# Kernel tuning notes

Measured on AMD Instinct MI355X. Metric: run time of the kernel, lower is better.

## Reference

```python
import jax, jax.numpy as jnp
import numpy as np

D_MODEL = 1024
NUM_HEADS = 16
D_HEAD = D_MODEL // NUM_HEADS


def setup_inputs() -> dict:
    key = jax.random.key(0)
    ks = jax.random.split(key, 9)
    s = 1.0 / np.sqrt(D_MODEL)
    inp = {"x": jax.random.normal(ks[0], (2, 2048, D_MODEL), dtype=jnp.float32)}
    for i, name in enumerate(["q", "k", "v", "o"]):
        inp[f"W_{name}"] = jax.random.uniform(ks[1 + 2 * i], (D_MODEL, D_MODEL), minval=-s, maxval=s, dtype=jnp.float32)
        inp[f"b_{name}"] = jax.random.uniform(ks[2 + 2 * i], (D_MODEL,), minval=-s, maxval=s, dtype=jnp.float32)
    return inp


def reference(x, W_q, b_q, W_k, b_k, W_v, b_v, W_o, b_o):
    B, S, _ = x.shape
    def heads(W, b):
        # [B,S,D] @ [D,D] -> [B,S,H,Dh] -> [B,H,S,Dh]
        return (x @ W.T + b).reshape(B, S, NUM_HEADS, D_HEAD).transpose(0, 2, 1, 3)
    Q, K, V = heads(W_q, b_q), heads(W_k, b_k), heads(W_v, b_v)
    scores = jnp.einsum("bhqd,bhkd->bhqk", Q, K) / jnp.sqrt(jnp.float32(D_HEAD))
    causal = jnp.tril(jnp.ones((S, S), dtype=bool))  # True = keep
    scores = jnp.where(causal, scores, -jnp.inf)
    A = jax.nn.softmax(scores, axis=-1)
    out = jnp.einsum("bhqk,bhkd->bhqd", A, V)  # [B,H,S,Dh]
    out = out.transpose(0, 2, 1, 3).reshape(B, S, D_MODEL)
    return out @ W_o.T + b_o
```

## Files before the change

### kernel.cpp

```cpp
#include <hip/hip_runtime.h>
#include <math.h>

#define D_MODEL 1024
#define NUM_HEADS 16
#define D_HEAD 64
#define SEQ 2048
#define BATCH 2
#define NROWS (BATCH * SEQ)

typedef short s8v __attribute__((ext_vector_type(8)));
typedef float f4v __attribute__((ext_vector_type(4)));

__device__ __forceinline__ short to_bf(float f) {
    union { float f; unsigned u; } x; x.f = f;
    unsigned r = x.u + 0x7fffu + ((x.u >> 16) & 1u);
    return (short)(r >> 16);
}

__device__ __forceinline__ void gld_lds16(const short* g, short* l) {
    __builtin_amdgcn_global_load_lds(
        (const __attribute__((address_space(1))) unsigned*)g,
        (__attribute__((address_space(3))) unsigned*)l, 16, 0, 0);
}

#define QSCALE 0.180336880f

__global__ __launch_bounds__(256) void cvt_fused(
    const float* __restrict__ x,  const float* __restrict__ Wq,
    const float* __restrict__ Wk, const float* __restrict__ Wv,
    const float* __restrict__ Wo,
    short* __restrict__ Xb, short* __restrict__ Wqkvb, short* __restrict__ Wob)
{
    const int NX = NROWS * D_MODEL / 4;
    const int NW = D_MODEL * D_MODEL / 4;
    int j = blockIdx.x * 256 + threadIdx.x;
    const float* src; short* dst; float sc = 1.f;
    if (j < NX)                 { src = x;  dst = Xb; }
    else if ((j -= NX) < NW)    { src = Wq; dst = Wqkvb; sc = QSCALE; }
    else if ((j -= NW) < NW)    { src = Wk; dst = Wqkvb + NW * 4; }
    else if ((j -= NW) < NW)    { src = Wv; dst = Wqkvb + NW * 8; }
    else                        { j -= NW; src = Wo; dst = Wob; }
    float4 v = ((const float4*)src)[j];
    short4 s = { to_bf(v.x * sc), to_bf(v.y * sc), to_bf(v.z * sc), to_bf(v.w * sc) };
    ((short4*)dst)[j] = s;
}

__global__ __launch_bounds__(256) void gemm_bf16(
    const short* __restrict__ Xb, const short* __restrict__ Wb,
    const float* __restrict__ B0, const float* __restrict__ B1, const float* __restrict__ B2,
    float* __restrict__ Ofp,
    short* __restrict__ Q0, short* __restrict__ K1, short* __restrict__ V2,
    int qkv_mode)
{
    __shared__ __align__(16) short smem[18432];
    short* As = smem;
    short* Bs = smem + 8192;

    const int t    = threadIdx.x;
    const int w    = t >> 6;
    const int lane = t & 63;
    const int quad = lane >> 4;
    const int l15  = lane & 15;
    const int wm   = w & 1, wn = w >> 1;

    const int n0 = blockIdx.x * 128;
    const int m0 = blockIdx.y * 128;

    f4v acc[4][4];
#pragma unroll
    for (int i = 0; i < 4; ++i)
#pragma unroll
        for (int j = 0; j < 4; ++j) acc[i][j] = (f4v){0.f, 0.f, 0.f, 0.f};

    for (int k0 = 0; k0 < D_MODEL; k0 += 64) {
#pragma unroll
        for (int i = 0; i < 4; ++i) {
            const int cid = i * 256 + t;
            const int row = cid >> 3, kc = cid & 7;
            gld_lds16(&Xb[(size_t)(m0 + row) * D_MODEL + k0 + kc * 8],
                      &As[(i * 256 + w * 64) * 8]);
            gld_lds16(&Wb[(size_t)(n0 + row) * D_MODEL + k0 + kc * 8],
                      &Bs[(i * 256 + w * 64) * 8]);
        }
        __syncthreads();

#pragma unroll
        for (int c = 0; c < 2; ++c) {
            s8v af[4], bf[4];
#pragma unroll
            for (int mi = 0; mi < 4; ++mi)
                af[mi] = *(const s8v*)&As[(wm * 64 + mi * 16 + l15) * 64 + c * 32 + quad * 8];
#pragma unroll
            for (int ni = 0; ni < 4; ++ni)
                bf[ni] = *(const s8v*)&Bs[(wn * 64 + ni * 16 + l15) * 64 + c * 32 + quad * 8];
#pragma unroll
            for (int mi = 0; mi < 4; ++mi)
#pragma unroll
                for (int ni = 0; ni < 4; ++ni)
                    acc[mi][ni] = __builtin_amdgcn_mfma_f32_16x16x32_bf16(
                        af[mi], bf[ni], acc[mi][ni], 0, 0, 0);
        }
        __syncthreads();
    }

    if (!qkv_mode) {
#pragma unroll
        for (int ni = 0; ni < 4; ++ni) {
            const int col = n0 + wn * 64 + ni * 16 + l15;
            const float bv = B0[col];
#pragma unroll
            for (int mi = 0; mi < 4; ++mi)
#pragma unroll
                for (int r = 0; r < 4; ++r) {
                    const int row = m0 + wm * 64 + mi * 16 + quad * 4 + r;
                    Ofp[(size_t)row * D_MODEL + col] = acc[mi][ni][r] + bv;
                }
        }
        return;
    }

    const int sel = n0 >> 10;
    const float* bias = sel == 0 ? B0 : sel == 1 ? B1 : B2;
    short* out        = sel == 0 ? Q0 : sel == 1 ? K1 : V2;
    const float bsc   = sel == 0 ? QSCALE : 1.f;
    const int h0 = (n0 & 1023) >> 6;

#pragma unroll
    for (int ni = 0; ni < 4; ++ni) {
        const int col = wn * 64 + ni * 16 + l15;
        const float bv = bias[(n0 & 1023) + col] * bsc;
#pragma unroll
        for (int mi = 0; mi < 4; ++mi)
#pragma unroll
            for (int r = 0; r < 4; ++r) {
                const int row = wm * 64 + mi * 16 + quad * 4 + r;
                const short v = to_bf(acc[mi][ni][r] + bv);
                if (sel < 2) smem[row * 144 + col] = v;
                else         smem[col * 144 + row] = v;
            }
    }
    __syncthreads();

    const int rr = t >> 1, half = t & 1;
    const int bb = m0 >> 11, mloc = m0 & (SEQ - 1);
    const short* src = &smem[rr * 144 + half * 64];
    short* dst;
    if (sel < 2)
        dst = out + (((size_t)(bb * NUM_HEADS + h0 + half) * SEQ + (mloc + rr)) * D_HEAD);
    else
        dst = out + ((size_t)(bb * NUM_HEADS + h0 + (rr >> 6)) * D_HEAD + (rr & 63)) * SEQ
                  + mloc + half * 64;
#pragma unroll
    for (int i = 0; i < 8; ++i)
        ((int4*)dst)[i] = ((const int4*)src)[i];
}

__global__ __launch_bounds__(256) void attn_mfma(
    const short* __restrict__ Qg, const short* __restrict__ Kg,
    const short* __restrict__ Vg, short* __restrict__ ctxb)
{
    __shared__ __align__(16) short Kb[128 * 64];
    __shared__ __align__(16) short Vs[64 * 128];
    __shared__ __align__(16) short Ps[4][32 * 72];
    __shared__ float lbuf[4][36];

    const int t    = threadIdx.x;
    const int w    = t >> 6;
    const int lane = t & 63;
    const int quad = lane >> 4;
    const int l15  = lane & 15;

    const int bidx = blockIdx.x;
    const int p    = bidx & 255;
    const int bh   = p >> 3;
    const int pair = p & 7;
    const int qt   = (bidx < 256) ? pair : 15 - pair;
    const int b    = bh >> 4, h = bh & 15;

    const short* qbase = Qg + (size_t)bh * SEQ * D_HEAD;
    const short* kbase = Kg + (size_t)bh * SEQ * D_HEAD;
    const short* vbase = Vg + (size_t)bh * D_HEAD * SEQ;
    const int q0 = qt * 128;
    const int qw = w * 32;

    s8v aq[2][2];
#pragma unroll
    for (int ns = 0; ns < 2; ++ns)
#pragma unroll
        for (int c = 0; c < 2; ++c)
            aq[ns][c] = *(const s8v*)&qbase[(size_t)(q0 + qw + ns * 16 + l15) * D_HEAD
                                            + c * 32 + quad * 8];

    f4v Oacc[2][4];
#pragma unroll
    for (int ms = 0; ms < 2; ++ms)
#pragma unroll
        for (int nt = 0; nt < 4; ++nt) Oacc[ms][nt] = (f4v){0.f, 0.f, 0.f, 0.f};
    float lsum[2] = {0.f, 0.f};

    for (int j = 0; j <= qt; ++j) {
        __syncthreads();
        {
            const int k0 = j * 128;
#pragma unroll
            for (int i = 0; i < 4; ++i) {
                const int cid = i * 256 + w * 64 + lane;
                {
                    const int row = cid >> 3, pp = cid & 7, g = pp ^ (row & 7);
                    gld_lds16(&kbase[(size_t)(k0 + row) * D_HEAD + g * 8],
                              &Kb[(i * 256 + w * 64) * 8]);
                }
                {
                    const int row = cid >> 4, pp = cid & 15;
                    const int g = (pp & 8) | ((pp & 7) ^ (row & 7));
                    gld_lds16(&vbase[(size_t)row * SEQ + k0 + g * 8],
                              &Vs[(i * 256 + w * 64) * 8]);
                }
            }
        }
        __syncthreads();

        const bool diag = (j == qt);

#pragma unroll
        for (int half = 0; half < 2; ++half) {
#pragma unroll
            for (int mt = 0; mt < 4; ++mt) {
                const int krow = half * 64 + mt * 16 + l15;
                s8v ka0 = *(const s8v*)&Kb[(krow * 8 + (quad ^ (l15 & 7))) * 8];
                s8v ka1 = *(const s8v*)&Kb[(krow * 8 + ((4 + quad) ^ (l15 & 7))) * 8];
#pragma unroll
                for (int ns = 0; ns < 2; ++ns) {
                    f4v st = (f4v){0.f, 0.f, 0.f, 0.f};
                    st = __builtin_amdgcn_mfma_f32_16x16x32_bf16(ka0, aq[ns][0], st, 0, 0, 0);
                    st = __builtin_amdgcn_mfma_f32_16x16x32_bf16(ka1, aq[ns][1], st, 0, 0, 0);
                    if (diag) {
#pragma unroll
                        for (int r = 0; r < 4; ++r)
                            if (half * 64 + mt * 16 + quad * 4 + r > qw + ns * 16 + l15)
                                st[r] = -INFINITY;
                    }
                    float e0 = exp2f(st[0]), e1 = exp2f(st[1]);
                    float e2 = exp2f(st[2]), e3 = exp2f(st[3]);
                    lsum[ns] += (e0 + e1) + (e2 + e3);
                    int2 pk;
                    pk.x = (int)((__float_as_uint(e0) >> 16) | (__float_as_uint(e1) & 0xffff0000u));
                    pk.y = (int)((__float_as_uint(e2) >> 16) | (__float_as_uint(e3) & 0xffff0000u));
                    *(int2*)&Ps[w][(ns * 16 + l15) * 72 + mt * 16 + quad * 4] = pk;
                }
            }
#pragma unroll
            for (int c2 = 0; c2 < 2; ++c2) {
                s8v ap0 = *(const s8v*)&Ps[w][l15 * 72 + c2 * 32 + quad * 8];
                s8v ap1 = *(const s8v*)&Ps[w][(16 + l15) * 72 + c2 * 32 + quad * 8];
                const int g = (half * 2 + c2) * 4 + quad;
                const int pos = (g & 8) | ((g & 7) ^ (l15 & 7));
                s8v bv[4];
#pragma unroll
                for (int nt = 0; nt < 4; ++nt)
                    bv[nt] = *(const s8v*)&Vs[((nt * 16 + l15) * 16 + pos) * 8];
#pragma unroll
                for (int nt = 0; nt < 4; ++nt) {
                    Oacc[0][nt] = __builtin_amdgcn_mfma_f32_16x16x32_bf16(
                        ap0, bv[nt], Oacc[0][nt], 0, 0, 0);
                    Oacc[1][nt] = __builtin_amdgcn_mfma_f32_16x16x32_bf16(
                        ap1, bv[nt], Oacc[1][nt], 0, 0, 0);
                }
            }
        }
    }

#pragma unroll
    for (int ns = 0; ns < 2; ++ns) {
        lsum[ns] += __shfl_xor(lsum[ns], 16, 64);
        lsum[ns] += __shfl_xor(lsum[ns], 32, 64);
    }
    if (quad == 0) { lbuf[w][l15] = lsum[0]; lbuf[w][16 + l15] = lsum[1]; }
#pragma unroll
    for (int ms = 0; ms < 2; ++ms) {
        float4 lv = *(float4*)&lbuf[w][ms * 16 + quad * 4];
        const float li[4] = {lv.x, lv.y, lv.z, lv.w};
#pragma unroll
        for (int r = 0; r < 4; ++r) {
            const float inv = 1.f / li[r];
            const int n = b * SEQ + q0 + qw + ms * 16 + quad * 4 + r;
            short* dst = &ctxb[(size_t)n * D_MODEL + h * D_HEAD + l15];
#pragma unroll
            for (int nt = 0; nt < 4; ++nt)
                dst[nt * 16] = to_bf(Oacc[ms][nt][r] * inv);
        }
    }
}

extern "C" void kernel_launch(void* const* d_in, const int* in_sizes, int n_in,
                              void* d_out, int out_size, void* d_ws, size_t ws_size,
                              hipStream_t stream)
{
    const float* x  = (const float*)d_in[0];
    const float* Wq = (const float*)d_in[1];
    const float* bq = (const float*)d_in[2];
    const float* Wk = (const float*)d_in[3];
    const float* bk = (const float*)d_in[4];
    const float* Wv = (const float*)d_in[5];
    const float* bv = (const float*)d_in[6];
    const float* Wo = (const float*)d_in[7];
    const float* bo = (const float*)d_in[8];
    float* out = (float*)d_out;

    short* wsp = (short*)d_ws;
    const size_t MAT = (size_t)NROWS * D_MODEL;
    short* Qb    = wsp;
    short* Kbg   = Qb + MAT;
    short* Vtb   = Kbg + MAT;
    short* ctxb  = Vtb + MAT;
    short* Xb    = ctxb + MAT;
    short* Wqkvb = Xb + MAT;
    short* Wob   = Wqkvb + 3 * D_MODEL * D_MODEL;

    cvt_fused<<<8192, 256, 0, stream>>>(x, Wq, Wk, Wv, Wo, Xb, Wqkvb, Wob);

    gemm_bf16<<<dim3(3 * D_MODEL / 128, NROWS / 128), 256, 0, stream>>>(
        Xb, Wqkvb, bq, bk, bv, nullptr, Qb, Kbg, Vtb, 1);

    attn_mfma<<<dim3(512), 256, 0, stream>>>(Qb, Kbg, Vtb, ctxb);

    gemm_bf16<<<dim3(D_MODEL / 128, NROWS / 128), 256, 0, stream>>>(
        ctxb, Wob, bo, bo, bo, out, nullptr, nullptr, nullptr, 0);
}
```

Before: 234.4 us.

## Split attention KV loop across two blocks and swizzle GEMM LDS tiles

The attention kernel now launches twice as many blocks. Each block handles every other 128-key tile (a two-way split over keys) and writes unnormalized bf16 partial outputs and row sums. A new combine kernel adds the two partials, normalizes them, and writes the context in the layout the output projection expects. Separately, the GEMM's LDS tiles get an XOR swizzle on the 16-byte chunk index to reduce bank conflicts on MFMA fragment reads. The split raises parallelism for the attention phase but adds an extra kernel launch, extra global traffic for the partials, and bf16 rounding of the partial sums.

```diff
diff --git a/kernel.cpp b/kernel.cpp
--- a/kernel.cpp
+++ b/kernel.cpp
@@ -76,10 +76,10 @@
 #pragma unroll
         for (int i = 0; i < 4; ++i) {
             const int cid = i * 256 + t;
-            const int row = cid >> 3, kc = cid & 7;
-            gld_lds16(&Xb[(size_t)(m0 + row) * D_MODEL + k0 + kc * 8],
+            const int row = cid >> 3, kc = cid & 7, g = kc ^ (row & 7);
+            gld_lds16(&Xb[(size_t)(m0 + row) * D_MODEL + k0 + g * 8],
                       &As[(i * 256 + w * 64) * 8]);
-            gld_lds16(&Wb[(size_t)(n0 + row) * D_MODEL + k0 + kc * 8],
+            gld_lds16(&Wb[(size_t)(n0 + row) * D_MODEL + k0 + g * 8],
                       &Bs[(i * 256 + w * 64) * 8]);
         }
         __syncthreads();
@@ -87,12 +87,13 @@
 #pragma unroll
         for (int c = 0; c < 2; ++c) {
             s8v af[4], bf[4];
+            const int pos = ((c * 4 + quad) ^ (l15 & 7)) * 8;
 #pragma unroll
             for (int mi = 0; mi < 4; ++mi)
-                af[mi] = *(const s8v*)&As[(wm * 64 + mi * 16 + l15) * 64 + c * 32 + quad * 8];
+                af[mi] = *(const s8v*)&As[(wm * 64 + mi * 16 + l15) * 64 + pos];
 #pragma unroll
             for (int ni = 0; ni < 4; ++ni)
-                bf[ni] = *(const s8v*)&Bs[(wn * 64 + ni * 16 + l15) * 64 + c * 32 + quad * 8];
+                bf[ni] = *(const s8v*)&Bs[(wn * 64 + ni * 16 + l15) * 64 + pos];
 #pragma unroll
             for (int mi = 0; mi < 4; ++mi)
 #pragma unroll
@@ -157,12 +158,12 @@
 
 __global__ __launch_bounds__(256) void attn_mfma(
     const short* __restrict__ Qg, const short* __restrict__ Kg,
-    const short* __restrict__ Vg, short* __restrict__ ctxb)
+    const short* __restrict__ Vg,
+    short* __restrict__ Op0, short* __restrict__ Op1, float* __restrict__ Lp)
 {
     __shared__ __align__(16) short Kb[128 * 64];
     __shared__ __align__(16) short Vs[64 * 128];
     __shared__ __align__(16) short Ps[4][32 * 72];
-    __shared__ float lbuf[4][36];
 
     const int t    = threadIdx.x;
     const int w    = t >> 6;
@@ -171,10 +172,11 @@
     const int l15  = lane & 15;
 
     const int bidx = blockIdx.x;
+    const int seg  = bidx >> 9;
     const int p    = bidx & 255;
     const int bh   = p >> 3;
     const int pair = p & 7;
-    const int qt   = (bidx < 256) ? pair : 15 - pair;
+    const int qt   = ((bidx >> 8) & 1) ? 15 - pair : pair;
     const int b    = bh >> 4, h = bh & 15;
 
     const short* qbase = Qg + (size_t)bh * SEQ * D_HEAD;
@@ -198,7 +200,7 @@
         for (int nt = 0; nt < 4; ++nt) Oacc[ms][nt] = (f4v){0.f, 0.f, 0.f, 0.f};
     float lsum[2] = {0.f, 0.f};
 
-    for (int j = 0; j <= qt; ++j) {
+    for (int j = seg; j <= qt; j += 2) {
         __syncthreads();
         {
             const int k0 = j * 128;
@@ -275,21 +277,51 @@
         lsum[ns] += __shfl_xor(lsum[ns], 16, 64);
         lsum[ns] += __shfl_xor(lsum[ns], 32, 64);
     }
-    if (quad == 0) { lbuf[w][l15] = lsum[0]; lbuf[w][16 + l15] = lsum[1]; }
-#pragma unroll
-    for (int ms = 0; ms < 2; ++ms) {
-        float4 lv = *(float4*)&lbuf[w][ms * 16 + quad * 4];
-        const float li[4] = {lv.x, lv.y, lv.z, lv.w};
+    float* L = Lp + ((size_t)seg << 16) + (size_t)bh * SEQ;
+    if (quad == 0) {
+        L[q0 + qw + l15]      = lsum[0];
+        L[q0 + qw + 16 + l15] = lsum[1];
+    }
+    short* Op = (seg ? Op1 : Op0) + (size_t)bh * SEQ * D_HEAD;
+#pragma unroll
+    for (int ms = 0; ms < 2; ++ms)
 #pragma unroll
         for (int r = 0; r < 4; ++r) {
-            const float inv = 1.f / li[r];
-            const int n = b * SEQ + q0 + qw + ms * 16 + quad * 4 + r;
-            short* dst = &ctxb[(size_t)n * D_MODEL + h * D_HEAD + l15];
+            const int nloc = q0 + qw + ms * 16 + quad * 4 + r;
+            short* dst = Op + (size_t)nloc * D_HEAD + l15;
 #pragma unroll
             for (int nt = 0; nt < 4; ++nt)
-                dst[nt * 16] = to_bf(Oacc[ms][nt][r] * inv);
-        }
-    }
+                dst[nt * 16] = to_bf(Oacc[ms][nt][r]);
+        }
+}
+
+__global__ __launch_bounds__(256) void combine(
+    const short* __restrict__ Op0, const short* __restrict__ Op1,
+    const float* __restrict__ Lp, short* __restrict__ ctxb)
+{
+    const int id  = blockIdx.x * 256 + threadIdx.x;
+    const int e   = id * 8;
+    const int bh  = e >> 17;
+    const int rem = e & 131071;
+    const int s   = rem >> 6, dh = rem & 63;
+    const int b   = bh >> 4,  h  = bh & 15;
+
+    int4 p0 = *(const int4*)&Op0[e];
+    int4 p1 = *(const int4*)&Op1[e];
+    const float inv = 1.f / (Lp[(size_t)bh * SEQ + s] + Lp[65536 + (size_t)bh * SEQ + s]);
+
+    const unsigned* u0 = (const unsigned*)&p0;
+    const unsigned* u1 = (const unsigned*)&p1;
+    short outv[8];
+#pragma unroll
+    for (int i = 0; i < 4; ++i) {
+        float a0 = __uint_as_float(u0[i] << 16), b0 = __uint_as_float(u0[i] & 0xffff0000u);
+        float a1 = __uint_as_float(u1[i] << 16), b1 = __uint_as_float(u1[i] & 0xffff0000u);
+        outv[2 * i]     = to_bf((a0 + a1) * inv);
+        outv[2 * i + 1] = to_bf((b0 + b1) * inv);
+    }
+    short* dst = &ctxb[(size_t)(b * SEQ + s) * D_MODEL + h * D_HEAD + dh];
+    *(int4*)dst = *(const int4*)outv;
 }
 
 extern "C" void kernel_launch(void* const* d_in, const int* in_sizes, int n_in,
@@ -316,13 +348,18 @@
     short* Xb    = ctxb + MAT;
     short* Wqkvb = Xb + MAT;
     short* Wob   = Wqkvb + 3 * D_MODEL * D_MODEL;
+    short* Op0   = Xb;
+    short* Op1   = Wob + D_MODEL * D_MODEL;
+    float* Lp    = (float*)(Op1 + MAT);
 
     cvt_fused<<<8192, 256, 0, stream>>>(x, Wq, Wk, Wv, Wo, Xb, Wqkvb, Wob);
 
     gemm_bf16<<<dim3(3 * D_MODEL / 128, NROWS / 128), 256, 0, stream>>>(
         Xb, Wqkvb, bq, bk, bv, nullptr, Qb, Kbg, Vtb, 1);
 
-    attn_mfma<<<dim3(512), 256, 0, stream>>>(Qb, Kbg, Vtb, ctxb);
+    attn_mfma<<<dim3(1024), 256, 0, stream>>>(Qb, Kbg, Vtb, Op0, Op1, Lp);
+
+    combine<<<dim3(2048), 256, 0, stream>>>(Op0, Op1, Lp, ctxb);
 
     gemm_bf16<<<dim3(D_MODEL / 128, NROWS / 128), 256, 0, stream>>>(
         ctxb, Wob, bo, bo, bo, out, nullptr, nullptr, nullptr, 0);
```

Result: faster. 215.5 us (-8.1%).
